# Kernel optimization log

Measured on AMD Instinct MI355X. Metric: run time of the kernel, lower is better.

The kernel has to match this reference:

```python
import jax, jax.numpy as jnp
import numpy as np


def _conv(x, w, stride):
    # Conv2d(k=3, stride, padding=1, bias=False), NCHW/OIHW
    return jax.lax.conv_general_dilated(
        x, w, (stride, stride), ((1, 1), (1, 1)),
        dimension_numbers=('NCHW', 'OIHW', 'NCHW'))


def _bn_silu(x, g, b, m, v):
    # BatchNorm2d (inference) + SiLU, fused elementwise
    scale = (g * jax.lax.rsqrt(v + 1e-5))[None, :, None, None]
    y = (x - m[None, :, None, None]) * scale + b[None, :, None, None]
    return y * jax.nn.sigmoid(y)


def _ss2d(x, in_w, dt_w, dt_b, B_w, C_w, A_log, D, out_w):
    # Low-rank 2D selective scan over flattened spatial tokens.
    Bn, C, H, W = x.shape
    L = H * W
    xt = x.reshape(Bn, C, L).transpose(0, 2, 1)            # [B,L,C]
    u = jnp.einsum('blc,rc->blr', xt, in_w)                # low-rank input [B,L,R]
    dt = jax.nn.softplus(jnp.einsum('blc,rc->blr', xt, dt_w) + dt_b)
    Bt = jnp.einsum('blc,nc->bln', xt, B_w)                # [B,L,N]
    Ct = jnp.einsum('blc,nc->bln', xt, C_w)                # [B,L,N]
    A = -jnp.exp(A_log)                                    # [R,N], stable (negative)

    def step(h, inp):
        u_t, dt_t, b_t, c_t = inp                          # [B,R],[B,R],[B,N],[B,N]
        dA = jnp.exp(dt_t[..., None] * A)                  # [B,R,N]
        h = dA * h + (dt_t[..., None] * b_t[:, None, :]) * u_t[..., None]
        y = jnp.einsum('brn,bn->br', h, c_t)               # [B,R]
        return h, (h, y)

    R, N = A_log.shape
    h0 = jnp.zeros((Bn, R, N), x.dtype)
    xs = (u.transpose(1, 0, 2), dt.transpose(1, 0, 2),
          Bt.transpose(1, 0, 2), Ct.transpose(1, 0, 2))
    _, (hs, ys) = jax.lax.scan(step, h0, xs)               # hs:[L,B,R,N] ys:[L,B,R]
    y = ys.transpose(1, 0, 2) + D * u                      # skip term D*u
    out = jnp.einsum('blr,cr->blc', y, out_w)              # project back to C
    x_out = (xt + out).transpose(0, 2, 1).reshape(Bn, C, H, W)
    state_seq = hs.transpose(1, 0, 2, 3)                   # [B,L,R,N]
    return x_out, state_seq


def setup_inputs() -> dict:
    key = jax.random.key(0)
    ks = jax.random.split(key, 24)
    f = jax.random.normal
    B, Cin, H, W = 8, 32, 112, 112
    E, R, N, NB = 64, 32, 64, 3
    inp = {}
    inp['x'] = f(ks[0], (B, Cin, H, W), jnp.float32)
    # stem
    inp['stem_w'] = f(ks[1], (E, Cin, 3, 3)) * 0.05
    inp['stem_g'] = 1.0 + 0.1 * f(ks[2], (E,))
    inp['stem_b'] = 0.1 * f(ks[3], (E,))
    inp['stem_m'] = 0.1 * f(ks[4], (E,))
    inp['stem_v'] = 1.0 + 0.1 * jax.random.uniform(ks[5], (E,))
    # SS2D blocks (stacked over num_blocks)
    inp['blk_in_w'] = f(ks[6], (NB, R, E)) * 0.1
    inp['blk_dt_w'] = f(ks[7], (NB, R, E)) * 0.05
    inp['blk_dt_b'] = f(ks[8], (NB, R)) * 0.1 - 2.0
    inp['blk_B_w'] = f(ks[9], (NB, N, E)) * 0.1
    inp['blk_C_w'] = f(ks[10], (NB, N, E)) * 0.1
    inp['blk_A_log'] = jnp.log(1.0 + jax.random.uniform(ks[11], (NB, R, N)) * 4.0)
    inp['blk_D'] = f(ks[12], (NB, R)) * 0.1
    inp['blk_out_w'] = f(ks[13], (NB, E, R)) * 0.1
    # down p4
    C4, C5 = 2 * E, 4 * E
    inp['p4_w'] = f(ks[14], (C4, E, 3, 3)) * 0.05
    inp['p4_g'] = 1.0 + 0.1 * f(ks[15], (C4,))
    inp['p4_b'] = 0.1 * f(ks[16], (C4,))
    inp['p4_m'] = 0.1 * f(ks[17], (C4,))
    inp['p4_v'] = 1.0 + 0.1 * jax.random.uniform(ks[18], (C4,))
    # down p5
    inp['p5_w'] = f(ks[19], (C5, C4, 3, 3)) * 0.05
    inp['p5_g'] = 1.0 + 0.1 * f(ks[20], (C5,))
    inp['p5_b'] = 0.1 * f(ks[21], (C5,))
    inp['p5_m'] = 0.1 * f(ks[22], (C5,))
    inp['p5_v'] = 1.0 + 0.1 * jax.random.uniform(ks[23], (C5,))
    return inp


def reference(x, stem_w, stem_g, stem_b, stem_m, stem_v,
              blk_in_w, blk_dt_w, blk_dt_b, blk_B_w, blk_C_w,
              blk_A_log, blk_D, blk_out_w,
              p4_w, p4_g, p4_b, p4_m, p4_v,
              p5_w, p5_g, p5_b, p5_m, p5_v):
    x = _bn_silu(_conv(x, stem_w, 2), stem_g, stem_b, stem_m, stem_v)
    states = []
    for i in range(blk_in_w.shape[0]):
        x, s = _ss2d(x, blk_in_w[i], blk_dt_w[i], blk_dt_b[i],
                     blk_B_w[i], blk_C_w[i], blk_A_log[i], blk_D[i], blk_out_w[i])
        states.append(s)
    p3 = x
    p4 = _bn_silu(_conv(p3, p4_w, 2), p4_g, p4_b, p4_m, p4_v)
    p5 = _bn_silu(_conv(p4, p5_w, 2), p5_g, p5_b, p5_m, p5_v)
    return (p3, p4, p5, jnp.stack(states))
```

## Files before the change

kernel.cpp:

```cpp
#include <hip/hip_runtime.h>
#include <cstdint>
#include <cstddef>

#define RFL(x) __builtin_amdgcn_readfirstlane(x)

constexpr int E  = 64;
constexpr int Rr = 32;
constexpr int Nn = 64;
constexpr int Lt = 3136;
constexpr int NC = 28;
constexpr int CL = 112;
constexpr int PD = 192;

__global__ __launch_bounds__(256) void k_setup(
    const float* __restrict__ in_w, const float* __restrict__ dt_w,
    const float* __restrict__ B_w, const float* __restrict__ C_w,
    const float* __restrict__ stem_w, const float* __restrict__ p4_w,
    const float* __restrict__ p5_w,
    float* __restrict__ wT, float* __restrict__ w3s,
    float* __restrict__ w34, float* __restrict__ w35) {
  int idx = blockIdx.x * 256 + threadIdx.x;
  if (idx < 36864) {
    int o = idx % PD; int c = (idx / PD) & 63; int i = idx / (PD * 64);
    float v;
    if (o < 32)       v = in_w[(i * 32 + o) * 64 + c];
    else if (o < 64)  v = dt_w[(i * 32 + (o - 32)) * 64 + c];
    else if (o < 128) v = B_w[(i * 64 + (o - 64)) * 64 + c];
    else              v = C_w[(i * 64 + (o - 128)) * 64 + c];
    wT[idx] = v;
  } else if (idx < 36864 + 18432) {
    int j = idx - 36864;
    int co = j % 64; int k = (j / 64) % 9; int ci = j / (64 * 9);
    w3s[j] = stem_w[((size_t)co * 32 + ci) * 9 + k];
  } else if (idx < 36864 + 18432 + 73728) {
    int j = idx - 36864 - 18432;
    int co = j % 128; int k = (j / 128) % 9; int ci = j / (128 * 9);
    w34[j] = p4_w[((size_t)co * 64 + ci) * 9 + k];
  } else if (idx < 36864 + 18432 + 73728 + 294912) {
    int j = idx - 36864 - 18432 - 73728;
    int co = j % 256; int k = (j / 256) % 9; int ci = j / (256 * 9);
    w35[j] = p5_w[((size_t)co * 128 + ci) * 9 + k];
  }
}

template<int CIN, int COUT, int HIN, int WIN>
__global__ __launch_bounds__(256) void k_conv(const float* __restrict__ x,
    const float* __restrict__ w3, const float* __restrict__ g, const float* __restrict__ bb,
    const float* __restrict__ m, const float* __restrict__ vv, float* __restrict__ out) {
  constexpr int HOUT = HIN / 2, WOUT = WIN / 2;
  constexpr int OWT = 7;
  constexpr int GWX = WOUT / OWT;
  constexpr int CIW = CIN / 4;
  __shared__ float xs[3][CIN][16];
  __shared__ float tbuf[4][64][8];

  int t = blockIdx.x;
  int b = t & 7; t >>= 3;
  int oh = t % HOUT; t /= HOUT;
  int gx = t % GWX; int cog = t / GWX;
  int lane = threadIdx.x & 63;
  int ws = RFL(threadIdx.x >> 6);
  int co = cog * 64 + lane;
  int iwb = gx * 14;
  int ih0 = oh * 2 - 1;

  for (int i = threadIdx.x; i < CIN * 3 * 16; i += 256) {
    int d = i & 15; int r3 = i >> 4;
    int kh = r3 / CIN; int ci = r3 & (CIN - 1);
    int iw = iwb + d - 1; int ih = ih0 + kh;
    float v = 0.f;
    if ((unsigned)iw < (unsigned)WIN && (unsigned)ih < (unsigned)HIN)
      v = x[(((size_t)(b * CIN + ci)) * HIN + ih) * WIN + iw];
    xs[kh][ci][d] = v;
  }
  __syncthreads();

  float acc[OWT];
#pragma unroll
  for (int o = 0; o < OWT; ++o) acc[o] = 0.f;

  int ci0 = ws * CIW;
#pragma unroll 2
  for (int cc = 0; cc < CIW; ++cc) {
    int ci = ci0 + cc;
    const float* wr = w3 + ((size_t)ci * 9) * COUT + co;
    float wk[9];
#pragma unroll
    for (int k = 0; k < 9; ++k) wk[k] = wr[(size_t)k * COUT];
#pragma unroll
    for (int kh = 0; kh < 3; ++kh) {
      const float4* tp4 = (const float4*)(&xs[kh][ci][0]);
      float4 q0 = tp4[0], q1 = tp4[1], q2 = tp4[2], q3 = tp4[3];
      float tp[16] = {q0.x, q0.y, q0.z, q0.w, q1.x, q1.y, q1.z, q1.w,
                      q2.x, q2.y, q2.z, q2.w, q3.x, q3.y, q3.z, q3.w};
#pragma unroll
      for (int o = 0; o < OWT; ++o) {
        acc[o] = fmaf(tp[2*o],     wk[kh*3+0], acc[o]);
        acc[o] = fmaf(tp[2*o + 1], wk[kh*3+1], acc[o]);
        acc[o] = fmaf(tp[2*o + 2], wk[kh*3+2], acc[o]);
      }
    }
  }
#pragma unroll
  for (int o = 0; o < OWT; ++o) tbuf[ws][lane][o] = acc[o];
  __syncthreads();

  for (int i = threadIdx.x; i < 64 * OWT; i += 256) {
    int cl = i / OWT, o = i - cl * OWT;
    float s = tbuf[0][cl][o] + tbuf[1][cl][o] + tbuf[2][cl][o] + tbuf[3][cl][o];
    int c2 = cog * 64 + cl;
    float scale = g[c2] * rsqrtf(vv[c2] + 1e-5f);
    float yv = (s - m[c2]) * scale + bb[c2];
    out[(((size_t)(b * COUT + c2)) * HOUT + oh) * WOUT + gx * OWT + o] =
        yv / (1.f + __expf(-yv));
  }
}

__global__ __launch_bounds__(256) void k_proj(const float* __restrict__ xin,
    const float* __restrict__ wT, const float* __restrict__ dt_b, float* __restrict__ P) {
  __shared__ float sm[64 * 196];
  int b = blockIdx.x & 7, tl = blockIdx.x >> 3;
  int l0 = tl * 64;
  int tid = threadIdx.x;
  for (int k = 0; k < 16; ++k) {
    int idx = k * 256 + tid; int c = idx >> 6, li = idx & 63;
    sm[c * 65 + li] = xin[(size_t)(b * 64 + c) * Lt + l0 + li];
  }
  __syncthreads();
  int tok = tid & 63;
  int og = RFL(tid >> 6);
  const float* wbase = wT + og * 48;
  float acc[48];
#pragma unroll
  for (int j = 0; j < 48; ++j) acc[j] = 0.f;
  for (int c = 0; c < 64; ++c) {
    float xv = sm[c * 65 + tok];
    const float4* w4 = (const float4*)(wbase + c * PD);
#pragma unroll
    for (int j = 0; j < 12; ++j) {
      float4 wv = __ldg(w4 + j);
      acc[4 * j + 0] = fmaf(xv, wv.x, acc[4 * j + 0]);
      acc[4 * j + 1] = fmaf(xv, wv.y, acc[4 * j + 1]);
      acc[4 * j + 2] = fmaf(xv, wv.z, acc[4 * j + 2]);
      acc[4 * j + 3] = fmaf(xv, wv.w, acc[4 * j + 3]);
    }
  }
  __syncthreads();
#pragma unroll
  for (int j = 0; j < 48; ++j) {
    int o = og * 48 + j;
    float v = acc[j];
    if (o >= 32 && o < 64) {
      v += dt_b[o - 32];
      v = fmaxf(v, 0.f) + log1pf(__expf(-fabsf(v)));
    }
    sm[tok * 196 + o] = v;
  }
  __syncthreads();
  float* dst = P + ((size_t)(b * Lt + l0)) * PD;
#pragma unroll
  for (int it = 0; it < 12; ++it) {
    int f = it * 1024 + tid * 4;
    int tk = f / 192;
    float4 v = *(const float4*)(&sm[tk * 196 + (f - tk * 192)]);
    *(float4*)(dst + f) = v;
  }
}

__global__ __launch_bounds__(256) void k_scan1(const float* __restrict__ P,
    const float* __restrict__ A_log, float* __restrict__ hfin, float* __restrict__ Pc) {
  __shared__ float xl[16][132];
  int bid = blockIdx.x;
  int b = bid & 7; int rest = bid >> 3;
  int c = rest % NC; int rg = rest / NC;
  int ws = RFL(threadIdx.x >> 6);
  int r = rg * 4 + ws;
  int n = threadIdx.x & 63;
  float a = -__expf(A_log[r * 64 + n]);
  const float* base = P + ((size_t)(b * Lt + c * CL)) * PD;
  int tl = threadIdx.x >> 4;
  int colb = (threadIdx.x & 15) * 8;
  float h = 0.f, sdt = 0.f;
  for (int s0 = 0; s0 < CL; s0 += 16) {
    __syncthreads();
    const float4* src = (const float4*)(base + (size_t)(s0 + tl) * PD + colb);
    float4 v0 = src[0], v1 = src[1];
    *(float4*)(&xl[tl][colb]) = v0;
    *(float4*)(&xl[tl][colb + 4]) = v1;
    __syncthreads();
#pragma unroll
    for (int tt = 0; tt < 16; ++tt) {
      float dt = xl[tt][32 + r];
      float u  = xl[tt][r];
      float bt = xl[tt][64 + n];
      h = fmaf(__expf(dt * a), h, (dt * u) * bt);
      sdt += dt;
    }
  }
  int o = ((b * 32 + r) * NC + c) * 64 + n;
  hfin[o] = h;
  Pc[o] = __expf(a * sdt);
}

__global__ __launch_bounds__(256) void k_scan3(const float* __restrict__ P,
    const float* __restrict__ A_log, const float* __restrict__ hfin,
    const float* __restrict__ Pcp, const float* __restrict__ Dp,
    float* __restrict__ states, float* __restrict__ y) {
  __shared__ float xl[16][196];
  __shared__ __align__(16) float ylds[4][16][68];
  int bid = blockIdx.x;
  int b = bid & 7; int rest = bid >> 3;
  int c = rest % NC; int rg = rest / NC;
  int ws = RFL(threadIdx.x >> 6);
  int r = rg * 4 + ws;
  int n = threadIdx.x & 63;
  float a = -__expf(A_log[r * 64 + n]);
  float Dr = Dp[r];
  const float* base = P + ((size_t)(b * Lt + c * CL)) * PD;
  float h = 0.f;
  {
    int bp = ((b * 32 + r) * NC) * 64 + n;
    for (int cc = 0; cc < c; ++cc)
      h = fmaf(Pcp[bp + cc * 64], h, hfin[bp + cc * 64]);
  }
  float* st = states + ((size_t)(b * Lt + c * CL) * 32 + r) * 64 + n;
  float* yrow = y + (size_t)(b * 32 + r) * Lt + c * CL;
  int tl = threadIdx.x >> 4;
  int colb = (threadIdx.x & 15) * 12;
  for (int s0 = 0; s0 < CL; s0 += 16) {
    __syncthreads();
    const float4* src = (const float4*)(base + (size_t)(s0 + tl) * PD + colb);
    float4 v0 = src[0], v1 = src[1], v2 = src[2];
    *(float4*)(&xl[tl][colb])     = v0;
    *(float4*)(&xl[tl][colb + 4]) = v1;
    *(float4*)(&xl[tl][colb + 8]) = v2;
    __syncthreads();
#pragma unroll
    for (int tt = 0; tt < 16; ++tt) {
      float dt = xl[tt][32 + r];
      float u  = xl[tt][r];
      float bt = xl[tt][64 + n];
      float ct = xl[tt][128 + n];
      h = fmaf(__expf(dt * a), h, (dt * u) * bt);
      __builtin_nontemporal_store(h, st + (size_t)(s0 + tt) * 2048);
      ylds[ws][tt][n] = h * ct;
    }
    if (n < 16) {
      const float4* rp = (const float4*)(&ylds[ws][n][0]);
      float a0 = 0.f, a1 = 0.f, a2 = 0.f, a3 = 0.f;
#pragma unroll
      for (int k = 0; k < 16; ++k) {
        float4 pv = rp[k];
        a0 += pv.x; a1 += pv.y; a2 += pv.z; a3 += pv.w;
      }
      float sum = (a0 + a1) + (a2 + a3);
      float uu = xl[n][r];
      yrow[s0 + n] = sum + Dr * uu;
    }
  }
}

__global__ __launch_bounds__(256) void k_outproj(const float* __restrict__ xin,
    const float* __restrict__ y, const float* __restrict__ ow, float* __restrict__ xout) {
  __shared__ float ylds[32 * 64];
  int b = blockIdx.x & 7, tl = blockIdx.x >> 3;
  int l0 = tl * 64;
  int tid = threadIdx.x;
  for (int k = 0; k < 8; ++k) {
    int idx = k * 256 + tid; int r = idx >> 6, li = idx & 63;
    ylds[r * 64 + li] = y[(size_t)(b * 32 + r) * Lt + l0 + li];
  }
  __syncthreads();
  int li = tid & 63, cg = RFL(tid >> 6);
  for (int cc = 0; cc < 16; ++cc) {
    int ci = cg * 16 + cc;
    float acc = xin[(size_t)(b * 64 + ci) * Lt + l0 + li];
    const float4* w4 = (const float4*)(ow + ci * 32);
#pragma unroll
    for (int r4 = 0; r4 < 8; ++r4) {
      float4 wv = __ldg(w4 + r4);
      acc = fmaf(ylds[(r4 * 4 + 0) * 64 + li], wv.x, acc);
      acc = fmaf(ylds[(r4 * 4 + 1) * 64 + li], wv.y, acc);
      acc = fmaf(ylds[(r4 * 4 + 2) * 64 + li], wv.z, acc);
      acc = fmaf(ylds[(r4 * 4 + 3) * 64 + li], wv.w, acc);
    }
    xout[(size_t)(b * 64 + ci) * Lt + l0 + li] = acc;
  }
}

extern "C" void kernel_launch(void* const* d_in, const int* in_sizes, int n_in,
                              void* d_out, int out_size, void* d_ws, size_t ws_size,
                              hipStream_t stream) {
  const float* x      = (const float*)d_in[0];
  const float* stem_w = (const float*)d_in[1];
  const float* stem_g = (const float*)d_in[2];
  const float* stem_b = (const float*)d_in[3];
  const float* stem_m = (const float*)d_in[4];
  const float* stem_v = (const float*)d_in[5];
  const float* in_w   = (const float*)d_in[6];
  const float* dt_w   = (const float*)d_in[7];
  const float* dt_b   = (const float*)d_in[8];
  const float* B_w    = (const float*)d_in[9];
  const float* C_w    = (const float*)d_in[10];
  const float* A_log  = (const float*)d_in[11];
  const float* Dp     = (const float*)d_in[12];
  const float* out_w  = (const float*)d_in[13];
  const float* p4_w   = (const float*)d_in[14];
  const float* p4_g   = (const float*)d_in[15];
  const float* p4_b   = (const float*)d_in[16];
  const float* p4_m   = (const float*)d_in[17];
  const float* p4_v   = (const float*)d_in[18];
  const float* p5_w   = (const float*)d_in[19];
  const float* p5_g   = (const float*)d_in[20];
  const float* p5_b   = (const float*)d_in[21];
  const float* p5_m   = (const float*)d_in[22];
  const float* p5_v   = (const float*)d_in[23];

  float* out = (float*)d_out;
  float* wsf = (float*)d_ws;

  float* p3out = out;
  float* p4out = out + 1605632;
  float* p5out = out + 2408448;
  float* stout = out + 2809856;

  float* x0    = wsf;
  float* x1    = wsf + 1605632;
  float* Pb    = wsf + 3211264;
  float* yb    = wsf + 8028160;
  float* hfin  = wsf + 8830976;
  float* Pc    = wsf + 9289728;
  float* wT    = wsf + 9748480;
  float* w3s   = wsf + 9785344;
  float* w34   = wsf + 9803776;
  float* w35   = wsf + 9877504;

  k_setup<<<1656, 256, 0, stream>>>(in_w, dt_w, B_w, C_w, stem_w, p4_w, p5_w,
                                    wT, w3s, w34, w35);

  k_conv<32, 64, 112, 112><<<3584, 256, 0, stream>>>(
      x, w3s, stem_g, stem_b, stem_m, stem_v, x0);

  const float* xi = x0;
  for (int i = 0; i < 3; ++i) {
    k_proj<<<392, 256, 0, stream>>>(xi, wT + i * 64 * PD, dt_b + i * 32, Pb);
    k_scan1<<<1792, 256, 0, stream>>>(Pb, A_log + i * 2048, hfin, Pc);
    k_scan3<<<1792, 256, 0, stream>>>(Pb, A_log + i * 2048, hfin, Pc, Dp + i * 32,
                                      stout + (size_t)i * 51380224, yb);
    float* dst = (i == 2) ? p3out : ((i == 0) ? x1 : x0);
    k_outproj<<<392, 256, 0, stream>>>(xi, yb, out_w + i * 2048, dst);
    xi = dst;
  }

  k_conv<64, 128, 56, 56><<<1792, 256, 0, stream>>>(
      p3out, w34, p4_g, p4_b, p4_m, p4_v, p4out);
  k_conv<128, 256, 28, 28><<<896, 256, 0, stream>>>(
      p4out, w35, p5_g, p5_b, p5_m, p5_v, p5out);
}
```

Baseline: 405.2 us.

## Rewrite strided convs as per-pixel threads with wave-uniform OIHW weight reads

Replaces the shared-memory tiled conv kernel, which split input channels across waves and reduced partial sums, with a kernel where each thread computes one output pixel for 8 output channels. Weights are read directly in OIHW layout with wave-uniform addresses, so the separate weight transpose for the convs is removed and the setup kernel only transposes projection weights. Inputs are loaded directly from global memory with stride-2 access instead of staged tiles, and for the smaller layers many lanes stay idle.

```diff
diff --git a/kernel.cpp b/kernel.cpp
--- a/kernel.cpp
+++ b/kernel.cpp
@@ -12,106 +12,70 @@
 constexpr int CL = 112;
 constexpr int PD = 192;
 
-__global__ __launch_bounds__(256) void k_setup(
-    const float* __restrict__ in_w, const float* __restrict__ dt_w,
-    const float* __restrict__ B_w, const float* __restrict__ C_w,
-    const float* __restrict__ stem_w, const float* __restrict__ p4_w,
-    const float* __restrict__ p5_w,
-    float* __restrict__ wT, float* __restrict__ w3s,
-    float* __restrict__ w34, float* __restrict__ w35) {
+__global__ __launch_bounds__(256) void k_wtrans(const float* __restrict__ in_w,
+    const float* __restrict__ dt_w, const float* __restrict__ B_w,
+    const float* __restrict__ C_w, float* __restrict__ wT) {
   int idx = blockIdx.x * 256 + threadIdx.x;
-  if (idx < 36864) {
-    int o = idx % PD; int c = (idx / PD) & 63; int i = idx / (PD * 64);
-    float v;
-    if (o < 32)       v = in_w[(i * 32 + o) * 64 + c];
-    else if (o < 64)  v = dt_w[(i * 32 + (o - 32)) * 64 + c];
-    else if (o < 128) v = B_w[(i * 64 + (o - 64)) * 64 + c];
-    else              v = C_w[(i * 64 + (o - 128)) * 64 + c];
-    wT[idx] = v;
-  } else if (idx < 36864 + 18432) {
-    int j = idx - 36864;
-    int co = j % 64; int k = (j / 64) % 9; int ci = j / (64 * 9);
-    w3s[j] = stem_w[((size_t)co * 32 + ci) * 9 + k];
-  } else if (idx < 36864 + 18432 + 73728) {
-    int j = idx - 36864 - 18432;
-    int co = j % 128; int k = (j / 128) % 9; int ci = j / (128 * 9);
-    w34[j] = p4_w[((size_t)co * 64 + ci) * 9 + k];
-  } else if (idx < 36864 + 18432 + 73728 + 294912) {
-    int j = idx - 36864 - 18432 - 73728;
-    int co = j % 256; int k = (j / 256) % 9; int ci = j / (256 * 9);
-    w35[j] = p5_w[((size_t)co * 128 + ci) * 9 + k];
-  }
-}
-
-template<int CIN, int COUT, int HIN, int WIN>
-__global__ __launch_bounds__(256) void k_conv(const float* __restrict__ x,
-    const float* __restrict__ w3, const float* __restrict__ g, const float* __restrict__ bb,
+  if (idx >= 3 * 64 * PD) return;
+  int o = idx % PD; int c = (idx / PD) & 63; int i = idx / (PD * 64);
+  float v;
+  if (o < 32)       v = in_w[(i * 32 + o) * 64 + c];
+  else if (o < 64)  v = dt_w[(i * 32 + (o - 32)) * 64 + c];
+  else if (o < 128) v = B_w[(i * 64 + (o - 64)) * 64 + c];
+  else              v = C_w[(i * 64 + (o - 128)) * 64 + c];
+  wT[idx] = v;
+}
+
+template<int CIN, int COUT, int HIN, int WIN, int RPW, int COT>
+__global__ __launch_bounds__(256) void k_conv5(const float* __restrict__ x,
+    const float* __restrict__ w, const float* __restrict__ g, const float* __restrict__ bb,
     const float* __restrict__ m, const float* __restrict__ vv, float* __restrict__ out) {
   constexpr int HOUT = HIN / 2, WOUT = WIN / 2;
-  constexpr int OWT = 7;
-  constexpr int GWX = WOUT / OWT;
-  constexpr int CIW = CIN / 4;
-  __shared__ float xs[3][CIN][16];
-  __shared__ float tbuf[4][64][8];
-
+  constexpr int RPB = 4 * RPW;
+  constexpr int OHG = (HOUT + RPB - 1) / RPB;
   int t = blockIdx.x;
   int b = t & 7; t >>= 3;
-  int oh = t % HOUT; t /= HOUT;
-  int gx = t % GWX; int cog = t / GWX;
-  int lane = threadIdx.x & 63;
-  int ws = RFL(threadIdx.x >> 6);
-  int co = cog * 64 + lane;
-  int iwb = gx * 14;
+  int ohg = t % OHG; int cog = t / OHG;
+  int wave = threadIdx.x >> 6, lane = threadIdx.x & 63;
+  if (lane >= RPW * WOUT) return;
+  int ohs = lane / WOUT, ow = lane - ohs * WOUT;
+  int oh = ohg * RPB + wave * RPW + ohs;
+  if (oh >= HOUT) return;
+  int co0 = cog * COT;
+  const float* xb = x + (size_t)b * CIN * HIN * WIN;
   int ih0 = oh * 2 - 1;
-
-  for (int i = threadIdx.x; i < CIN * 3 * 16; i += 256) {
-    int d = i & 15; int r3 = i >> 4;
-    int kh = r3 / CIN; int ci = r3 & (CIN - 1);
-    int iw = iwb + d - 1; int ih = ih0 + kh;
-    float v = 0.f;
-    if ((unsigned)iw < (unsigned)WIN && (unsigned)ih < (unsigned)HIN)
-      v = x[(((size_t)(b * CIN + ci)) * HIN + ih) * WIN + iw];
-    xs[kh][ci][d] = v;
-  }
-  __syncthreads();
-
-  float acc[OWT];
-#pragma unroll
-  for (int o = 0; o < OWT; ++o) acc[o] = 0.f;
-
-  int ci0 = ws * CIW;
+  int iw = ow * 2;
+  float acc[COT];
+#pragma unroll
+  for (int j = 0; j < COT; ++j) acc[j] = 0.f;
 #pragma unroll 2
-  for (int cc = 0; cc < CIW; ++cc) {
-    int ci = ci0 + cc;
-    const float* wr = w3 + ((size_t)ci * 9) * COUT + co;
-    float wk[9];
-#pragma unroll
-    for (int k = 0; k < 9; ++k) wk[k] = wr[(size_t)k * COUT];
+  for (int ci = 0; ci < CIN; ++ci) {
+    const float* xp = xb + (size_t)ci * HIN * WIN;
+    float tp[3][3];
 #pragma unroll
     for (int kh = 0; kh < 3; ++kh) {
-      const float4* tp4 = (const float4*)(&xs[kh][ci][0]);
-      float4 q0 = tp4[0], q1 = tp4[1], q2 = tp4[2], q3 = tp4[3];
-      float tp[16] = {q0.x, q0.y, q0.z, q0.w, q1.x, q1.y, q1.z, q1.w,
-                      q2.x, q2.y, q2.z, q2.w, q3.x, q3.y, q3.z, q3.w};
-#pragma unroll
-      for (int o = 0; o < OWT; ++o) {
-        acc[o] = fmaf(tp[2*o],     wk[kh*3+0], acc[o]);
-        acc[o] = fmaf(tp[2*o + 1], wk[kh*3+1], acc[o]);
-        acc[o] = fmaf(tp[2*o + 2], wk[kh*3+2], acc[o]);
-      }
-    }
-  }
-#pragma unroll
-  for (int o = 0; o < OWT; ++o) tbuf[ws][lane][o] = acc[o];
-  __syncthreads();
-
-  for (int i = threadIdx.x; i < 64 * OWT; i += 256) {
-    int cl = i / OWT, o = i - cl * OWT;
-    float s = tbuf[0][cl][o] + tbuf[1][cl][o] + tbuf[2][cl][o] + tbuf[3][cl][o];
-    int c2 = cog * 64 + cl;
+      int ih = ih0 + kh;
+      bool rok = (unsigned)ih < (unsigned)HIN;
+      const float* xr = xp + (size_t)ih * WIN;
+      tp[kh][0] = (rok && ow > 0) ? xr[iw - 1] : 0.f;
+      tp[kh][1] = rok ? xr[iw] : 0.f;
+      tp[kh][2] = rok ? xr[iw + 1] : 0.f;
+    }
+    const float* wc = w + (size_t)(co0 * CIN + ci) * 9;
+#pragma unroll
+    for (int j = 0; j < COT; ++j) {
+      const float* wj = wc + (size_t)j * CIN * 9;
+#pragma unroll
+      for (int k = 0; k < 9; ++k)
+        acc[j] = fmaf(tp[k / 3][k % 3], wj[k], acc[j]);
+    }
+  }
+#pragma unroll
+  for (int j = 0; j < COT; ++j) {
+    int c2 = co0 + j;
     float scale = g[c2] * rsqrtf(vv[c2] + 1e-5f);
-    float yv = (s - m[c2]) * scale + bb[c2];
-    out[(((size_t)(b * COUT + c2)) * HOUT + oh) * WOUT + gx * OWT + o] =
+    float yv = (acc[j] - m[c2]) * scale + bb[c2];
+    out[(((size_t)(b * COUT + c2)) * HOUT + oh) * WOUT + ow] =
         yv / (1.f + __expf(-yv));
   }
 }
@@ -331,15 +295,11 @@
   float* hfin  = wsf + 8830976;
   float* Pc    = wsf + 9289728;
   float* wT    = wsf + 9748480;
-  float* w3s   = wsf + 9785344;
-  float* w34   = wsf + 9803776;
-  float* w35   = wsf + 9877504;
-
-  k_setup<<<1656, 256, 0, stream>>>(in_w, dt_w, B_w, C_w, stem_w, p4_w, p5_w,
-                                    wT, w3s, w34, w35);
-
-  k_conv<32, 64, 112, 112><<<3584, 256, 0, stream>>>(
-      x, w3s, stem_g, stem_b, stem_m, stem_v, x0);
+
+  k_wtrans<<<144, 256, 0, stream>>>(in_w, dt_w, B_w, C_w, wT);
+
+  k_conv5<32, 64, 112, 112, 1, 8><<<896, 256, 0, stream>>>(
+      x, stem_w, stem_g, stem_b, stem_m, stem_v, x0);
 
   const float* xi = x0;
   for (int i = 0; i < 3; ++i) {
@@ -352,8 +312,8 @@
     xi = dst;
   }
 
-  k_conv<64, 128, 56, 56><<<1792, 256, 0, stream>>>(
-      p3out, w34, p4_g, p4_b, p4_m, p4_v, p4out);
-  k_conv<128, 256, 28, 28><<<896, 256, 0, stream>>>(
-      p4out, w35, p5_g, p5_b, p5_m, p5_v, p5out);
-}
+  k_conv5<64, 128, 56, 56, 2, 8><<<512, 256, 0, stream>>>(
+      p3out, p4_w, p4_g, p4_b, p4_m, p4_v, p4out);
+  k_conv5<128, 256, 28, 28, 4, 8><<<256, 256, 0, stream>>>(
+      p4out, p5_w, p5_g, p5_b, p5_m, p5_v, p5out);
+}
```

New measurement: 521.1 us. 1.29x slower.
